# Kernel optimization log

Measured on AMD Instinct MI355X. Metric: run time of the kernel, lower is better.

Reference implementation:

```python
import jax, jax.numpy as jnp
import numpy as np

D_MODEL = 1024
N_HEADS = 16
D_K = D_MODEL // N_HEADS
MAX_POS = 512          # max_position_embeddings; att_span = pos_ebd_size
ATT_SPAN = MAX_POS
B, T = 4, 1024
SCALE_FACTOR = 3       # 1 + c2p + p2c


def setup_inputs() -> dict:
    key = jax.random.key(0)
    ks = jax.random.split(key, 16)
    init = lambda k, shape: (jax.random.normal(k, shape, dtype=jnp.float32) * 0.02)
    inp = {
        "x": jax.random.normal(ks[0], (B, T, D_MODEL), dtype=jnp.float32),
        "Wq": init(ks[1], (D_MODEL, D_MODEL)), "bq": jnp.zeros((D_MODEL,), jnp.float32),
        "Wk": init(ks[2], (D_MODEL, D_MODEL)), "bk": jnp.zeros((D_MODEL,), jnp.float32),
        "Wv": init(ks[3], (D_MODEL, D_MODEL)), "bv": jnp.zeros((D_MODEL,), jnp.float32),
        "Wo": init(ks[4], (D_MODEL, D_MODEL)), "bo": jnp.zeros((D_MODEL,), jnp.float32),
        "Wpk": init(ks[5], (D_MODEL, D_MODEL)), "bpk": jnp.zeros((D_MODEL,), jnp.float32),
        "Wpq": init(ks[6], (D_MODEL, D_MODEL)), "bpq": jnp.zeros((D_MODEL,), jnp.float32),
        "rel_emb": init(ks[7], (2 * ATT_SPAN, D_MODEL)),
    }
    return inp


def _heads(y):
    # (B,T,D) -> (B,H,T,d_k)
    b, t, _ = y.shape
    return y.reshape(b, t, N_HEADS, D_K).transpose(0, 2, 1, 3)


def reference(x, Wq, bq, Wk, bk, Wv, bv, Wo, bo, Wpk, bpk, Wpq, bpq, rel_emb):
    b, t, c = x.shape
    scale = 1.0 / jnp.sqrt(jnp.asarray(D_K * SCALE_FACTOR, x.dtype))

    Q = _heads(x @ Wq.T + bq)  # (B,H,T,d)
    K = _heads(x @ Wk.T + bk)
    V = _heads(x @ Wv.T + bv)

    # relative_position[q,k] = k - q ; rel_pos = clamp(rel + span, 0, 2*span-1)
    rel = jnp.arange(t)[None, :] - jnp.arange(t)[:, None]          # (T,T)
    rel_pos = jnp.clip(rel + ATT_SPAN, 0, 2 * ATT_SPAN - 1)        # c2p index
    p2c_pos = jnp.clip(-rel + ATT_SPAN, 0, 2 * ATT_SPAN - 1)       # p2c index

    # content-to-content
    scores = jnp.einsum('bhqd,bhkd->bhqk', Q, K) * scale

    # c2p: pos_key (2S,H,d) -> per-head scores against Q, then gather over rel_pos
    pos_key = (rel_emb @ Wpk.T + bpk).reshape(2 * ATT_SPAN, N_HEADS, D_K)
    c2p = jnp.einsum('bhqd,shd->bhqs', Q, pos_key) * scale          # (B,H,T,2S)
    c2p = jnp.take_along_axis(c2p, rel_pos[None, None, :, :], axis=-1)  # (B,H,T,T)

    # p2c: pos_query scores against K, gather with p2c_pos, transpose q<->k
    pos_query = (rel_emb @ Wpq.T + bpq).reshape(2 * ATT_SPAN, N_HEADS, D_K)
    p2c = jnp.einsum('bhkd,shd->bhks', K, pos_query) * scale        # (B,H,T,2S)
    p2c = jnp.take_along_axis(p2c, p2c_pos[None, None, :, :], axis=-1)  # (B,H,k,q)
    p2c = jnp.swapaxes(p2c, -1, -2)                                 # (B,H,q,k)

    scores = scores + c2p + p2c
    probs = jax.nn.softmax(scores, axis=-1)
    ctx = jnp.einsum('bhqk,bhkd->bhqd', probs, V)
    ctx = ctx.transpose(0, 2, 1, 3).reshape(b, t, c)
    return ctx @ Wo.T + bo
```

## Files before the change

kernel.cpp:

```cpp
#include <hip/hip_runtime.h>
#include <stdint.h>

typedef __attribute__((ext_vector_type(8))) short bf16x8;
typedef __attribute__((ext_vector_type(4))) float f32x4;

#define DM   1024
#define TT   1024
#define NH   16
#define DKH  64
#define SPAN 512
#define S2   1024
#define MT   4096

__device__ __forceinline__ unsigned short f2b(float f) {
  unsigned int u = __builtin_bit_cast(unsigned int, f);
  u = (u + 0x7FFFu + ((u >> 16) & 1u)) >> 16;
  return (unsigned short)u;
}
__device__ __forceinline__ float b2f(unsigned short h) {
  unsigned int u = ((unsigned int)h) << 16;
  return __builtin_bit_cast(float, u);
}

__device__ __forceinline__ int swz(int row, int col) {
  return (row << 6) + ((((col >> 3) ^ (row & 7)) << 3) | (col & 7));
}

struct CvtArgs {
  const float* src[8];
  unsigned short* dst[8];
  int n[8];
};
__global__ void cvt_multi(CvtArgs a) {
  const int ti = blockIdx.y;
  const float* __restrict__ in = a.src[ti];
  unsigned short* __restrict__ out = a.dst[ti];
  const int n = a.n[ti];
  int i = (blockIdx.x * blockDim.x + threadIdx.x) * 4;
  int stride = gridDim.x * blockDim.x * 4;
  for (; i < n; i += stride) {
    float4 v = *(const float4*)(in + i);
    ushort4 o;
    o.x = f2b(v.x); o.y = f2b(v.y); o.z = f2b(v.z); o.w = f2b(v.w);
    *(ushort4*)(out + i) = o;
  }
}

__global__ __launch_bounds__(256) void gemm_bt(
    const unsigned short* __restrict__ A, const unsigned short* __restrict__ B,
    const float* __restrict__ bias0, const float* __restrict__ bias1, const float* __restrict__ bias2,
    void* __restrict__ C,
    int M, int N, int K, int lda, int ldb, int ldc,
    long long sA, long long sB, long long sC,
    float a0, float a1, float a2, int modes)
{
  __shared__ unsigned short Al[128 * 72];
  __shared__ unsigned short Bl[128 * 72];
  const int t = threadIdx.x;
  const int w = t >> 6, l = t & 63;
  const int g = l >> 4, li = l & 15;
  const int wr = w >> 1, wc = w & 1;
  const int row0 = blockIdx.x * 128, col0 = blockIdx.y * 128;
  const int z = blockIdx.z;
  const unsigned short* Ab = A + (long long)z * sA;
  const unsigned short* Bb = B + (long long)z * sB;

  f32x4 acc[4][4];
#pragma unroll
  for (int m = 0; m < 4; m++)
#pragma unroll
    for (int n = 0; n < 4; n++) acc[m][n] = (f32x4){0.f, 0.f, 0.f, 0.f};

  for (int k0 = 0; k0 < K; k0 += 64) {
    __syncthreads();
#pragma unroll
    for (int i = 0; i < 4; i++) {
      int c = t + 256 * i;
      int r = c >> 3, c8 = (c & 7) * 8;
      *(bf16x8*)&Al[r * 72 + c8] = *(const bf16x8*)&Ab[(long long)(row0 + r) * lda + k0 + c8];
      *(bf16x8*)&Bl[r * 72 + c8] = *(const bf16x8*)&Bb[(long long)(col0 + r) * ldb + k0 + c8];
    }
    __syncthreads();
#pragma unroll
    for (int kk = 0; kk < 2; kk++) {
      bf16x8 af[4], bfr[4];
#pragma unroll
      for (int m = 0; m < 4; m++) af[m]  = *(bf16x8*)&Al[(wr * 64 + m * 16 + li) * 72 + kk * 32 + g * 8];
#pragma unroll
      for (int n = 0; n < 4; n++) bfr[n] = *(bf16x8*)&Bl[(wc * 64 + n * 16 + li) * 72 + kk * 32 + g * 8];
#pragma unroll
      for (int m = 0; m < 4; m++)
#pragma unroll
        for (int n = 0; n < 4; n++)
          acc[m][n] = __builtin_amdgcn_mfma_f32_16x16x32_bf16(af[m], bfr[n], acc[m][n], 0, 0, 0);
    }
  }

  const float alpha = z == 0 ? a0 : (z == 1 ? a1 : a2);
  const float* bias = z == 0 ? bias0 : (z == 1 ? bias1 : bias2);
  const int mode = (modes >> (4 * z)) & 15;
  const long long zoff = (long long)z * sC;

#pragma unroll
  for (int m = 0; m < 4; m++) {
    int row = row0 + wr * 64 + m * 16 + g * 4;
#pragma unroll
    for (int n = 0; n < 4; n++) {
      int col = col0 + wc * 64 + n * 16 + li;
      float bv = bias ? bias[col] : 0.0f;
      if (mode == 2) {
        ushort4 st;
        st.x = f2b((acc[m][n][0] + bv) * alpha);
        st.y = f2b((acc[m][n][1] + bv) * alpha);
        st.z = f2b((acc[m][n][2] + bv) * alpha);
        st.w = f2b((acc[m][n][3] + bv) * alpha);
        *(ushort4*)&((unsigned short*)C)[zoff + (long long)col * M + row] = st;
      } else {
#pragma unroll
        for (int r = 0; r < 4; r++) {
          float v = (acc[m][n][r] + bv) * alpha;
          long long idx = zoff + (long long)(row + r) * ldc + col;
          if (mode == 1) ((unsigned short*)C)[idx] = f2b(v);
          else           ((float*)C)[idx] = v;
        }
      }
    }
  }
}

__global__ __launch_bounds__(256, 3) void attn_fused(
    const unsigned short* __restrict__ Qb, const unsigned short* __restrict__ Kb,
    const unsigned short* __restrict__ VT,
    const unsigned short* __restrict__ PKb, const unsigned short* __restrict__ PQb,
    unsigned short* __restrict__ ctxb)
{
  __shared__ unsigned short Kl[64 * 64];
  __shared__ unsigned short Vtl[64 * 64];
  __shared__ unsigned short Ct[128 * 64];
  __shared__ unsigned short Pq[128 * 64];

  const int t = threadIdx.x, w = t >> 6, l = t & 63, g = l >> 4, li = l & 15;
  const int bid = blockIdx.x;
  const int role = (bid & 7) * 128 + (bid >> 3);
  const int q0 = (role & 15) * 64;
  const int h = (role >> 4) & 15;
  const int b = role >> 8;
  const long long qkbase = ((long long)b * TT) * DM + h * DKH;
  const long long vtb = (long long)(h * DKH) * MT + (long long)b * TT;
  const int hbase = h * DKH;

  bf16x8 aq[2];
#pragma unroll
  for (int kk = 0; kk < 2; kk++)
    aq[kk] = *(const bf16x8*)&Qb[qkbase + (long long)(q0 + w * 16 + li) * DM + kk * 32 + g * 8];

  int w0 = SPAN - q0 - 64;
  w0 = w0 < 0 ? 0 : (w0 > S2 - 128 ? S2 - 128 : w0);
#pragma unroll
  for (int i = 0; i < 4; i++) {
    int c = t + 256 * i;
    int jr = c >> 3, c8 = (c & 7) * 8;
    *(bf16x8*)&Ct[swz((w0 + jr) & 127, c8)] =
        *(const bf16x8*)&PKb[(long long)(w0 + jr) * DM + hbase + c8];
  }
  __syncthreads();
  {
    f32x4 cp[8];
#pragma unroll
    for (int jb = 0; jb < 8; jb++) cp[jb] = (f32x4){0.f, 0.f, 0.f, 0.f};
    __builtin_amdgcn_s_setprio(1);
#pragma unroll
    for (int kk = 0; kk < 2; kk++)
#pragma unroll
      for (int jb = 0; jb < 8; jb++) {
        bf16x8 pkf = *(bf16x8*)&Ct[swz(jb * 16 + li, kk * 32 + g * 8)];
        cp[jb] = __builtin_amdgcn_mfma_f32_16x16x32_bf16(aq[kk], pkf, cp[jb], 0, 0, 0);
      }
    __builtin_amdgcn_s_setprio(0);
    __syncthreads();
#pragma unroll
    for (int jb = 0; jb < 8; jb++) {
      ushort4 a;
      a.x = f2b(cp[jb][0]); a.y = f2b(cp[jb][1]);
      a.z = f2b(cp[jb][2]); a.w = f2b(cp[jb][3]);
      *(ushort4*)&Ct[swz(jb * 16 + li, w * 16 + g * 4)] = a;
    }
  }

  f32x4 o[4];
#pragma unroll
  for (int n = 0; n < 4; n++) o[n] = (f32x4){0.f, 0.f, 0.f, 0.f};
  float mrow[4], lrow[4];
#pragma unroll
  for (int r = 0; r < 4; r++) { mrow[r] = -1e30f; lrow[r] = 0.f; }

  for (int kt = 0; kt < TT / 64; kt++) {
    const int k0 = kt * 64;
    const int d0 = k0 - q0 + SPAN;
    int w0n = d0 - 64;
    w0n = w0n < 0 ? 0 : (w0n > S2 - 128 ? S2 - 128 : w0n);
    const bool slide = (w0n != w0);
    const int sb = w0 & 127;
    const int newrow0 = w0 + 128;
    w0 = w0n;

    __syncthreads();
#pragma unroll
    for (int i = 0; i < 2; i++) {
      int c = t + 256 * i;
      int r = c >> 3, c8 = (c & 7) * 8;
      *(bf16x8*)&Kl[swz(r, c8)]  = *(const bf16x8*)&Kb[qkbase + (long long)(k0 + r) * DM + c8];
      *(bf16x8*)&Vtl[swz(r, c8)] = *(const bf16x8*)&VT[vtb + (long long)r * MT + k0 + c8];
    }
#pragma unroll
    for (int i = 0; i < 4; i++) {
      int c = t + 256 * i;
      int jr = c >> 3, c8 = (c & 7) * 8;
      *(bf16x8*)&Pq[swz(jr, c8)] = *(const bf16x8*)&PQb[(long long)(w0 + jr) * DM + hbase + c8];
    }
    if (slide) {
#pragma unroll
      for (int i = 0; i < 2; i++) {
        int c = t + 256 * i;
        int jr = c >> 3, c8 = (c & 7) * 8;
        *(bf16x8*)&Ct[swz(sb + jr, c8)] =
            *(const bf16x8*)&PKb[(long long)(newrow0 + jr) * DM + hbase + c8];
      }
    }
    __syncthreads();

    bf16x8 ak[2];
#pragma unroll
    for (int kk = 0; kk < 2; kk++) ak[kk] = *(bf16x8*)&Kl[swz(w * 16 + li, kk * 32 + g * 8)];

    __builtin_amdgcn_s_setprio(1);
    f32x4 sc[4];
#pragma unroll
    for (int f = 0; f < 4; f++) sc[f] = (f32x4){0.f, 0.f, 0.f, 0.f};
#pragma unroll
    for (int kk = 0; kk < 2; kk++)
#pragma unroll
      for (int f = 0; f < 4; f++) {
        bf16x8 bk = *(bf16x8*)&Kl[swz(f * 16 + li, kk * 32 + g * 8)];
        sc[f] = __builtin_amdgcn_mfma_f32_16x16x32_bf16(aq[kk], bk, sc[f], 0, 0, 0);
      }
    f32x4 cp2[4];
#pragma unroll
    for (int jb = 0; jb < 4; jb++) cp2[jb] = (f32x4){0.f, 0.f, 0.f, 0.f};
    if (slide) {
#pragma unroll
      for (int kk = 0; kk < 2; kk++)
#pragma unroll
        for (int jb = 0; jb < 4; jb++) {
          bf16x8 pkf = *(bf16x8*)&Ct[swz(sb + jb * 16 + li, kk * 32 + g * 8)];
          cp2[jb] = __builtin_amdgcn_mfma_f32_16x16x32_bf16(aq[kk], pkf, cp2[jb], 0, 0, 0);
        }
    }
    int loA = d0 + w * 16 - 63; loA = loA < w0 ? w0 : loA;
    int hiA = d0 + w * 16 + 15; hiA = hiA > w0 + 127 ? w0 + 127 : hiA;
    const int jb_lo = (loA - w0) >> 4;
    const int jb_n  = ((hiA - w0) >> 4) - jb_lo;
    f32x4 pp[6];
#pragma unroll
    for (int u = 0; u < 6; u++) pp[u] = (f32x4){0.f, 0.f, 0.f, 0.f};
#pragma unroll
    for (int kk = 0; kk < 2; kk++)
#pragma unroll
      for (int u = 0; u < 6; u++)
        if (u <= jb_n) {
          bf16x8 pqf = *(bf16x8*)&Pq[swz((jb_lo + u) * 16 + li, kk * 32 + g * 8)];
          pp[u] = __builtin_amdgcn_mfma_f32_16x16x32_bf16(ak[kk], pqf, pp[u], 0, 0, 0);
        }
    __builtin_amdgcn_s_setprio(0);
    __syncthreads();

    if (slide) {
#pragma unroll
      for (int jb = 0; jb < 4; jb++) {
        ushort4 a;
        a.x = f2b(cp2[jb][0]); a.y = f2b(cp2[jb][1]);
        a.z = f2b(cp2[jb][2]); a.w = f2b(cp2[jb][3]);
        *(ushort4*)&Ct[swz(sb + jb * 16 + li, w * 16 + g * 4)] = a;
      }
    }
#pragma unroll
    for (int u = 0; u < 6; u++)
      if (u <= jb_n) {
        ushort4 a;
        a.x = f2b(pp[u][0]); a.y = f2b(pp[u][1]);
        a.z = f2b(pp[u][2]); a.w = f2b(pp[u][3]);
        *(ushort4*)&Pq[swz((jb_lo + u) * 16 + li, w * 16 + g * 4)] = a;
      }
    __syncthreads();

    float p[4][4];
    float tmax[4] = {-1e30f, -1e30f, -1e30f, -1e30f};
#pragma unroll
    for (int f = 0; f < 4; f++)
#pragma unroll
      for (int r = 0; r < 4; r++) {
        int qi = w * 16 + g * 4 + r;
        int ki = f * 16 + li;
        int sraw = d0 + ki - qi;
        int scl = sraw < 0 ? 0 : (sraw > S2 - 1 ? S2 - 1 : sraw);
        int slot = scl & 127;
        int j = scl - w0;
        float v = sc[f][r] + b2f(Ct[swz(slot, qi)]) + b2f(Pq[swz(j, ki)]);
        p[f][r] = v;
        tmax[r] = fmaxf(tmax[r], v);
      }
#pragma unroll
    for (int msk = 1; msk <= 8; msk <<= 1)
#pragma unroll
      for (int r = 0; r < 4; r++) tmax[r] = fmaxf(tmax[r], __shfl_xor(tmax[r], msk));
    float corr[4];
#pragma unroll
    for (int r = 0; r < 4; r++) {
      float mn = fmaxf(mrow[r], tmax[r]);
      corr[r] = __expf(mrow[r] - mn);
      mrow[r] = mn;
      lrow[r] *= corr[r];
    }
#pragma unroll
    for (int n = 0; n < 4; n++)
#pragma unroll
      for (int r = 0; r < 4; r++) o[n][r] *= corr[r];

    float ps[4] = {0.f, 0.f, 0.f, 0.f};
#pragma unroll
    for (int f = 0; f < 4; f++)
#pragma unroll
      for (int r = 0; r < 4; r++) {
        float e = __expf(p[f][r] - mrow[r]);
        ps[r] += e;
        Kl[swz(w * 16 + g * 4 + r, f * 16 + li)] = f2b(e);
      }
#pragma unroll
    for (int msk = 1; msk <= 8; msk <<= 1)
#pragma unroll
      for (int r = 0; r < 4; r++) ps[r] += __shfl_xor(ps[r], msk);
#pragma unroll
    for (int r = 0; r < 4; r++) lrow[r] += ps[r];

    __builtin_amdgcn_s_setprio(1);
#pragma unroll
    for (int kk = 0; kk < 2; kk++) {
      bf16x8 ap = *(bf16x8*)&Kl[swz(w * 16 + li, kk * 32 + g * 8)];
#pragma unroll
      for (int n = 0; n < 4; n++) {
        bf16x8 bvf = *(bf16x8*)&Vtl[swz(n * 16 + li, kk * 32 + g * 8)];
        o[n] = __builtin_amdgcn_mfma_f32_16x16x32_bf16(ap, bvf, o[n], 0, 0, 0);
      }
    }
    __builtin_amdgcn_s_setprio(0);
  }

#pragma unroll
  for (int n = 0; n < 4; n++)
#pragma unroll
    for (int r = 0; r < 4; r++) {
      int q = q0 + w * 16 + g * 4 + r;
      float val = o[n][r] / lrow[r];
      ctxb[((long long)b * TT + q) * DM + h * DKH + n * 16 + li] = f2b(val);
    }
}

extern "C" void kernel_launch(void* const* d_in, const int* in_sizes, int n_in,
                              void* d_out, int out_size, void* d_ws, size_t ws_size,
                              hipStream_t stream) {
  const float* x   = (const float*)d_in[0];
  const float* Wq  = (const float*)d_in[1];
  const float* bq  = (const float*)d_in[2];
  const float* Wk  = (const float*)d_in[3];
  const float* bk  = (const float*)d_in[4];
  const float* Wv  = (const float*)d_in[5];
  const float* bv  = (const float*)d_in[6];
  const float* Wo  = (const float*)d_in[7];
  const float* bo  = (const float*)d_in[8];
  const float* Wpk = (const float*)d_in[9];
  const float* bpk = (const float*)d_in[10];
  const float* Wpq = (const float*)d_in[11];
  const float* bpq = (const float*)d_in[12];
  const float* rel = (const float*)d_in[13];

  uint8_t* ws = (uint8_t*)d_ws;
  size_t off = 0;
  auto alloc = [&](size_t bytes) -> void* {
    void* p = ws + off;
    off += (bytes + 255) & ~(size_t)255;
    return p;
  };
  unsigned short* xb   = (unsigned short*)alloc((size_t)MT * DM * 2);
  unsigned short* Wqb  = (unsigned short*)alloc((size_t)DM * DM * 2);
  unsigned short* Wkb  = (unsigned short*)alloc((size_t)DM * DM * 2);
  unsigned short* Wvb  = (unsigned short*)alloc((size_t)DM * DM * 2);
  unsigned short* Wob  = (unsigned short*)alloc((size_t)DM * DM * 2);
  unsigned short* Wpkb = (unsigned short*)alloc((size_t)DM * DM * 2);
  unsigned short* Wpqb = (unsigned short*)alloc((size_t)DM * DM * 2);
  unsigned short* reb  = (unsigned short*)alloc((size_t)S2 * DM * 2);
  unsigned short* Qb   = (unsigned short*)alloc((size_t)MT * DM * 2);
  unsigned short* Kb   = (unsigned short*)alloc((size_t)MT * DM * 2);
  unsigned short* VT   = (unsigned short*)alloc((size_t)MT * DM * 2);
  unsigned short* PKb  = (unsigned short*)alloc((size_t)S2 * DM * 2);
  unsigned short* PQb  = (unsigned short*)alloc((size_t)S2 * DM * 2);
  unsigned short* ctxb = (unsigned short*)alloc((size_t)MT * DM * 2);

  const float scale = 0.07216878364870323f;

  CvtArgs ca;
  ca.src[0] = x;   ca.dst[0] = xb;   ca.n[0] = MT * DM;
  ca.src[1] = Wq;  ca.dst[1] = Wqb;  ca.n[1] = DM * DM;
  ca.src[2] = Wk;  ca.dst[2] = Wkb;  ca.n[2] = DM * DM;
  ca.src[3] = Wv;  ca.dst[3] = Wvb;  ca.n[3] = DM * DM;
  ca.src[4] = Wo;  ca.dst[4] = Wob;  ca.n[4] = DM * DM;
  ca.src[5] = Wpk; ca.dst[5] = Wpkb; ca.n[5] = DM * DM;
  ca.src[6] = Wpq; ca.dst[6] = Wpqb; ca.n[6] = DM * DM;
  ca.src[7] = rel; ca.dst[7] = reb;  ca.n[7] = S2 * DM;
  cvt_multi<<<dim3(1024, 8), dim3(256), 0, stream>>>(ca);

  gemm_bt<<<dim3(MT / 128, DM / 128, 3), dim3(256), 0, stream>>>(
      xb, Wqb, bq, bk, bv, Qb,
      MT, DM, DM, DM, DM, DM,
      0, (long long)DM * DM, (long long)MT * DM,
      scale, 1.0f, 1.0f, 0x211);

  gemm_bt<<<dim3(S2 / 128, DM / 128, 2), dim3(256), 0, stream>>>(
      reb, Wpkb, bpk, bpq, nullptr, PKb,
      S2, DM, DM, DM, DM, DM,
      0, (long long)DM * DM, (long long)S2 * DM,
      1.0f, scale, 1.0f, 0x11);

  attn_fused<<<dim3(1024), dim3(256), 0, stream>>>(
      Qb, Kb, VT, PKb, PQb, ctxb);

  gemm_bt<<<dim3(MT / 128, DM / 128, 1), dim3(256), 0, stream>>>(
      ctxb, Wob, bo, nullptr, nullptr, d_out,
      MT, DM, DM, DM, DM, DM,
      0, 0, 0,
      1.0f, 1.0f, 1.0f, 0x0);
}
```

Before: 262.0 us.

## Make attention kernel persistent with atomic work queue and fold log2e into scale

The attention kernel now launches 768 persistent blocks that take their first tile from blockIdx and later tiles from a global atomic counter, which the conversion kernel resets before use. The intent is to smooth out the tail imbalance caused by tiles that do different amounts of sliding-window work. Separately, log2(e) is folded into the Q and position-projection scales so softmax can use exp2f instead of __expf. The queue adds an atomic and an extra barrier per tile, and it depends on the counter being reset by an earlier launch on the same stream.

```diff
diff --git a/kernel.cpp b/kernel.cpp
--- a/kernel.cpp
+++ b/kernel.cpp
@@ -31,7 +31,8 @@
   unsigned short* dst[8];
   int n[8];
 };
-__global__ void cvt_multi(CvtArgs a) {
+__global__ void cvt_multi(CvtArgs a, unsigned int* counter) {
+  if (blockIdx.x == 0 && blockIdx.y == 0 && threadIdx.x == 0) *counter = 768u;
   const int ti = blockIdx.y;
   const float* __restrict__ in = a.src[ti];
   unsigned short* __restrict__ out = a.dst[ti];
@@ -132,237 +133,249 @@
     const unsigned short* __restrict__ Qb, const unsigned short* __restrict__ Kb,
     const unsigned short* __restrict__ VT,
     const unsigned short* __restrict__ PKb, const unsigned short* __restrict__ PQb,
-    unsigned short* __restrict__ ctxb)
+    unsigned short* __restrict__ ctxb, unsigned int* __restrict__ counter)
 {
   __shared__ unsigned short Kl[64 * 64];
   __shared__ unsigned short Vtl[64 * 64];
   __shared__ unsigned short Ct[128 * 64];
   __shared__ unsigned short Pq[128 * 64];
+  __shared__ unsigned int role_sh;
 
   const int t = threadIdx.x, w = t >> 6, l = t & 63, g = l >> 4, li = l & 15;
-  const int bid = blockIdx.x;
-  const int role = (bid & 7) * 128 + (bid >> 3);
-  const int q0 = (role & 15) * 64;
-  const int h = (role >> 4) & 15;
-  const int b = role >> 8;
-  const long long qkbase = ((long long)b * TT) * DM + h * DKH;
-  const long long vtb = (long long)(h * DKH) * MT + (long long)b * TT;
-  const int hbase = h * DKH;
-
-  bf16x8 aq[2];
-#pragma unroll
-  for (int kk = 0; kk < 2; kk++)
-    aq[kk] = *(const bf16x8*)&Qb[qkbase + (long long)(q0 + w * 16 + li) * DM + kk * 32 + g * 8];
-
-  int w0 = SPAN - q0 - 64;
-  w0 = w0 < 0 ? 0 : (w0 > S2 - 128 ? S2 - 128 : w0);
-#pragma unroll
-  for (int i = 0; i < 4; i++) {
-    int c = t + 256 * i;
-    int jr = c >> 3, c8 = (c & 7) * 8;
-    *(bf16x8*)&Ct[swz((w0 + jr) & 127, c8)] =
-        *(const bf16x8*)&PKb[(long long)(w0 + jr) * DM + hbase + c8];
-  }
-  __syncthreads();
-  {
-    f32x4 cp[8];
-#pragma unroll
-    for (int jb = 0; jb < 8; jb++) cp[jb] = (f32x4){0.f, 0.f, 0.f, 0.f};
-    __builtin_amdgcn_s_setprio(1);
+
+  unsigned int idx = blockIdx.x;
+  bool first = true;
+
+  for (;;) {
+    if (!first && t == 0) role_sh = atomicAdd(counter, 1u);
+    __syncthreads();
+    if (!first) idx = role_sh;
+    if (idx >= 1024u) break;
+    first = false;
+
+    const int role = (idx & 7) * 128 + (int)(idx >> 3);
+    const int q0 = (role & 15) * 64;
+    const int h = (role >> 4) & 15;
+    const int b = role >> 8;
+    const long long qkbase = ((long long)b * TT) * DM + h * DKH;
+    const long long vtb = (long long)(h * DKH) * MT + (long long)b * TT;
+    const int hbase = h * DKH;
+
+    bf16x8 aq[2];
 #pragma unroll
     for (int kk = 0; kk < 2; kk++)
-#pragma unroll
-      for (int jb = 0; jb < 8; jb++) {
-        bf16x8 pkf = *(bf16x8*)&Ct[swz(jb * 16 + li, kk * 32 + g * 8)];
-        cp[jb] = __builtin_amdgcn_mfma_f32_16x16x32_bf16(aq[kk], pkf, cp[jb], 0, 0, 0);
-      }
-    __builtin_amdgcn_s_setprio(0);
-    __syncthreads();
-#pragma unroll
-    for (int jb = 0; jb < 8; jb++) {
-      ushort4 a;
-      a.x = f2b(cp[jb][0]); a.y = f2b(cp[jb][1]);
-      a.z = f2b(cp[jb][2]); a.w = f2b(cp[jb][3]);
-      *(ushort4*)&Ct[swz(jb * 16 + li, w * 16 + g * 4)] = a;
-    }
-  }
-
-  f32x4 o[4];
-#pragma unroll
-  for (int n = 0; n < 4; n++) o[n] = (f32x4){0.f, 0.f, 0.f, 0.f};
-  float mrow[4], lrow[4];
-#pragma unroll
-  for (int r = 0; r < 4; r++) { mrow[r] = -1e30f; lrow[r] = 0.f; }
-
-  for (int kt = 0; kt < TT / 64; kt++) {
-    const int k0 = kt * 64;
-    const int d0 = k0 - q0 + SPAN;
-    int w0n = d0 - 64;
-    w0n = w0n < 0 ? 0 : (w0n > S2 - 128 ? S2 - 128 : w0n);
-    const bool slide = (w0n != w0);
-    const int sb = w0 & 127;
-    const int newrow0 = w0 + 128;
-    w0 = w0n;
-
-    __syncthreads();
-#pragma unroll
-    for (int i = 0; i < 2; i++) {
-      int c = t + 256 * i;
-      int r = c >> 3, c8 = (c & 7) * 8;
-      *(bf16x8*)&Kl[swz(r, c8)]  = *(const bf16x8*)&Kb[qkbase + (long long)(k0 + r) * DM + c8];
-      *(bf16x8*)&Vtl[swz(r, c8)] = *(const bf16x8*)&VT[vtb + (long long)r * MT + k0 + c8];
-    }
+      aq[kk] = *(const bf16x8*)&Qb[qkbase + (long long)(q0 + w * 16 + li) * DM + kk * 32 + g * 8];
+
+    int w0 = SPAN - q0 - 64;
+    w0 = w0 < 0 ? 0 : (w0 > S2 - 128 ? S2 - 128 : w0);
 #pragma unroll
     for (int i = 0; i < 4; i++) {
       int c = t + 256 * i;
       int jr = c >> 3, c8 = (c & 7) * 8;
-      *(bf16x8*)&Pq[swz(jr, c8)] = *(const bf16x8*)&PQb[(long long)(w0 + jr) * DM + hbase + c8];
-    }
-    if (slide) {
+      *(bf16x8*)&Ct[swz((w0 + jr) & 127, c8)] =
+          *(const bf16x8*)&PKb[(long long)(w0 + jr) * DM + hbase + c8];
+    }
+    __syncthreads();
+    {
+      f32x4 cp[8];
+#pragma unroll
+      for (int jb = 0; jb < 8; jb++) cp[jb] = (f32x4){0.f, 0.f, 0.f, 0.f};
+      __builtin_amdgcn_s_setprio(1);
+#pragma unroll
+      for (int kk = 0; kk < 2; kk++)
+#pragma unroll
+        for (int jb = 0; jb < 8; jb++) {
+          bf16x8 pkf = *(bf16x8*)&Ct[swz(jb * 16 + li, kk * 32 + g * 8)];
+          cp[jb] = __builtin_amdgcn_mfma_f32_16x16x32_bf16(aq[kk], pkf, cp[jb], 0, 0, 0);
+        }
+      __builtin_amdgcn_s_setprio(0);
+      __syncthreads();
+#pragma unroll
+      for (int jb = 0; jb < 8; jb++) {
+        ushort4 a;
+        a.x = f2b(cp[jb][0]); a.y = f2b(cp[jb][1]);
+        a.z = f2b(cp[jb][2]); a.w = f2b(cp[jb][3]);
+        *(ushort4*)&Ct[swz(jb * 16 + li, w * 16 + g * 4)] = a;
+      }
+    }
+
+    f32x4 o[4];
+#pragma unroll
+    for (int n = 0; n < 4; n++) o[n] = (f32x4){0.f, 0.f, 0.f, 0.f};
+    float mrow[4], lrow[4];
+#pragma unroll
+    for (int r = 0; r < 4; r++) { mrow[r] = -1e30f; lrow[r] = 0.f; }
+
+    for (int kt = 0; kt < TT / 64; kt++) {
+      const int k0 = kt * 64;
+      const int d0 = k0 - q0 + SPAN;
+      int w0n = d0 - 64;
+      w0n = w0n < 0 ? 0 : (w0n > S2 - 128 ? S2 - 128 : w0n);
+      const bool slide = (w0n != w0);
+      const int sb = w0 & 127;
+      const int newrow0 = w0 + 128;
+      w0 = w0n;
+
+      __syncthreads();
 #pragma unroll
       for (int i = 0; i < 2; i++) {
         int c = t + 256 * i;
+        int r = c >> 3, c8 = (c & 7) * 8;
+        *(bf16x8*)&Kl[swz(r, c8)]  = *(const bf16x8*)&Kb[qkbase + (long long)(k0 + r) * DM + c8];
+        *(bf16x8*)&Vtl[swz(r, c8)] = *(const bf16x8*)&VT[vtb + (long long)r * MT + k0 + c8];
+      }
+#pragma unroll
+      for (int i = 0; i < 4; i++) {
+        int c = t + 256 * i;
         int jr = c >> 3, c8 = (c & 7) * 8;
-        *(bf16x8*)&Ct[swz(sb + jr, c8)] =
-            *(const bf16x8*)&PKb[(long long)(newrow0 + jr) * DM + hbase + c8];
-      }
-    }
-    __syncthreads();
-
-    bf16x8 ak[2];
-#pragma unroll
-    for (int kk = 0; kk < 2; kk++) ak[kk] = *(bf16x8*)&Kl[swz(w * 16 + li, kk * 32 + g * 8)];
-
-    __builtin_amdgcn_s_setprio(1);
-    f32x4 sc[4];
-#pragma unroll
-    for (int f = 0; f < 4; f++) sc[f] = (f32x4){0.f, 0.f, 0.f, 0.f};
-#pragma unroll
-    for (int kk = 0; kk < 2; kk++)
-#pragma unroll
-      for (int f = 0; f < 4; f++) {
-        bf16x8 bk = *(bf16x8*)&Kl[swz(f * 16 + li, kk * 32 + g * 8)];
-        sc[f] = __builtin_amdgcn_mfma_f32_16x16x32_bf16(aq[kk], bk, sc[f], 0, 0, 0);
-      }
-    f32x4 cp2[4];
-#pragma unroll
-    for (int jb = 0; jb < 4; jb++) cp2[jb] = (f32x4){0.f, 0.f, 0.f, 0.f};
-    if (slide) {
+        *(bf16x8*)&Pq[swz(jr, c8)] = *(const bf16x8*)&PQb[(long long)(w0 + jr) * DM + hbase + c8];
+      }
+      if (slide) {
+#pragma unroll
+        for (int i = 0; i < 2; i++) {
+          int c = t + 256 * i;
+          int jr = c >> 3, c8 = (c & 7) * 8;
+          *(bf16x8*)&Ct[swz(sb + jr, c8)] =
+              *(const bf16x8*)&PKb[(long long)(newrow0 + jr) * DM + hbase + c8];
+        }
+      }
+      __syncthreads();
+
+      bf16x8 ak[2];
+#pragma unroll
+      for (int kk = 0; kk < 2; kk++) ak[kk] = *(bf16x8*)&Kl[swz(w * 16 + li, kk * 32 + g * 8)];
+
+      __builtin_amdgcn_s_setprio(1);
+      f32x4 sc[4];
+#pragma unroll
+      for (int f = 0; f < 4; f++) sc[f] = (f32x4){0.f, 0.f, 0.f, 0.f};
 #pragma unroll
       for (int kk = 0; kk < 2; kk++)
 #pragma unroll
+        for (int f = 0; f < 4; f++) {
+          bf16x8 bk = *(bf16x8*)&Kl[swz(f * 16 + li, kk * 32 + g * 8)];
+          sc[f] = __builtin_amdgcn_mfma_f32_16x16x32_bf16(aq[kk], bk, sc[f], 0, 0, 0);
+        }
+      f32x4 cp2[4];
+#pragma unroll
+      for (int jb = 0; jb < 4; jb++) cp2[jb] = (f32x4){0.f, 0.f, 0.f, 0.f};
+      if (slide) {
+#pragma unroll
+        for (int kk = 0; kk < 2; kk++)
+#pragma unroll
+          for (int jb = 0; jb < 4; jb++) {
+            bf16x8 pkf = *(bf16x8*)&Ct[swz(sb + jb * 16 + li, kk * 32 + g * 8)];
+            cp2[jb] = __builtin_amdgcn_mfma_f32_16x16x32_bf16(aq[kk], pkf, cp2[jb], 0, 0, 0);
+          }
+      }
+      int loA = d0 + w * 16 - 63; loA = loA < w0 ? w0 : loA;
+      int hiA = d0 + w * 16 + 15; hiA = hiA > w0 + 127 ? w0 + 127 : hiA;
+      const int jb_lo = (loA - w0) >> 4;
+      const int jb_n  = ((hiA - w0) >> 4) - jb_lo;
+      f32x4 pp[6];
+#pragma unroll
+      for (int u = 0; u < 6; u++) pp[u] = (f32x4){0.f, 0.f, 0.f, 0.f};
+#pragma unroll
+      for (int kk = 0; kk < 2; kk++)
+#pragma unroll
+        for (int u = 0; u < 6; u++)
+          if (u <= jb_n) {
+            bf16x8 pqf = *(bf16x8*)&Pq[swz((jb_lo + u) * 16 + li, kk * 32 + g * 8)];
+            pp[u] = __builtin_amdgcn_mfma_f32_16x16x32_bf16(ak[kk], pqf, pp[u], 0, 0, 0);
+          }
+      __builtin_amdgcn_s_setprio(0);
+      __syncthreads();
+
+      if (slide) {
+#pragma unroll
         for (int jb = 0; jb < 4; jb++) {
-          bf16x8 pkf = *(bf16x8*)&Ct[swz(sb + jb * 16 + li, kk * 32 + g * 8)];
-          cp2[jb] = __builtin_amdgcn_mfma_f32_16x16x32_bf16(aq[kk], pkf, cp2[jb], 0, 0, 0);
-        }
-    }
-    int loA = d0 + w * 16 - 63; loA = loA < w0 ? w0 : loA;
-    int hiA = d0 + w * 16 + 15; hiA = hiA > w0 + 127 ? w0 + 127 : hiA;
-    const int jb_lo = (loA - w0) >> 4;
-    const int jb_n  = ((hiA - w0) >> 4) - jb_lo;
-    f32x4 pp[6];
-#pragma unroll
-    for (int u = 0; u < 6; u++) pp[u] = (f32x4){0.f, 0.f, 0.f, 0.f};
-#pragma unroll
-    for (int kk = 0; kk < 2; kk++)
+          ushort4 a;
+          a.x = f2b(cp2[jb][0]); a.y = f2b(cp2[jb][1]);
+          a.z = f2b(cp2[jb][2]); a.w = f2b(cp2[jb][3]);
+          *(ushort4*)&Ct[swz(sb + jb * 16 + li, w * 16 + g * 4)] = a;
+        }
+      }
 #pragma unroll
       for (int u = 0; u < 6; u++)
         if (u <= jb_n) {
-          bf16x8 pqf = *(bf16x8*)&Pq[swz((jb_lo + u) * 16 + li, kk * 32 + g * 8)];
-          pp[u] = __builtin_amdgcn_mfma_f32_16x16x32_bf16(ak[kk], pqf, pp[u], 0, 0, 0);
-        }
-    __builtin_amdgcn_s_setprio(0);
-    __syncthreads();
-
-    if (slide) {
-#pragma unroll
-      for (int jb = 0; jb < 4; jb++) {
-        ushort4 a;
-        a.x = f2b(cp2[jb][0]); a.y = f2b(cp2[jb][1]);
-        a.z = f2b(cp2[jb][2]); a.w = f2b(cp2[jb][3]);
-        *(ushort4*)&Ct[swz(sb + jb * 16 + li, w * 16 + g * 4)] = a;
-      }
-    }
-#pragma unroll
-    for (int u = 0; u < 6; u++)
-      if (u <= jb_n) {
-        ushort4 a;
-        a.x = f2b(pp[u][0]); a.y = f2b(pp[u][1]);
-        a.z = f2b(pp[u][2]); a.w = f2b(pp[u][3]);
-        *(ushort4*)&Pq[swz((jb_lo + u) * 16 + li, w * 16 + g * 4)] = a;
-      }
-    __syncthreads();
-
-    float p[4][4];
-    float tmax[4] = {-1e30f, -1e30f, -1e30f, -1e30f};
-#pragma unroll
-    for (int f = 0; f < 4; f++)
+          ushort4 a;
+          a.x = f2b(pp[u][0]); a.y = f2b(pp[u][1]);
+          a.z = f2b(pp[u][2]); a.w = f2b(pp[u][3]);
+          *(ushort4*)&Pq[swz((jb_lo + u) * 16 + li, w * 16 + g * 4)] = a;
+        }
+      __syncthreads();
+
+      float p[4][4];
+      float tmax[4] = {-1e30f, -1e30f, -1e30f, -1e30f};
+#pragma unroll
+      for (int f = 0; f < 4; f++)
+#pragma unroll
+        for (int r = 0; r < 4; r++) {
+          int qi = w * 16 + g * 4 + r;
+          int ki = f * 16 + li;
+          int sraw = d0 + ki - qi;
+          int scl = sraw < 0 ? 0 : (sraw > S2 - 1 ? S2 - 1 : sraw);
+          int slot = scl & 127;
+          int j = scl - w0;
+          float v = sc[f][r] + b2f(Ct[swz(slot, qi)]) + b2f(Pq[swz(j, ki)]);
+          p[f][r] = v;
+          tmax[r] = fmaxf(tmax[r], v);
+        }
+#pragma unroll
+      for (int msk = 1; msk <= 8; msk <<= 1)
+#pragma unroll
+        for (int r = 0; r < 4; r++) tmax[r] = fmaxf(tmax[r], __shfl_xor(tmax[r], msk));
+      float corr[4];
 #pragma unroll
       for (int r = 0; r < 4; r++) {
-        int qi = w * 16 + g * 4 + r;
-        int ki = f * 16 + li;
-        int sraw = d0 + ki - qi;
-        int scl = sraw < 0 ? 0 : (sraw > S2 - 1 ? S2 - 1 : sraw);
-        int slot = scl & 127;
-        int j = scl - w0;
-        float v = sc[f][r] + b2f(Ct[swz(slot, qi)]) + b2f(Pq[swz(j, ki)]);
-        p[f][r] = v;
-        tmax[r] = fmaxf(tmax[r], v);
-      }
-#pragma unroll
-    for (int msk = 1; msk <= 8; msk <<= 1)
-#pragma unroll
-      for (int r = 0; r < 4; r++) tmax[r] = fmaxf(tmax[r], __shfl_xor(tmax[r], msk));
-    float corr[4];
-#pragma unroll
-    for (int r = 0; r < 4; r++) {
-      float mn = fmaxf(mrow[r], tmax[r]);
-      corr[r] = __expf(mrow[r] - mn);
-      mrow[r] = mn;
-      lrow[r] *= corr[r];
-    }
+        float mn = fmaxf(mrow[r], tmax[r]);
+        corr[r] = exp2f(mrow[r] - mn);
+        mrow[r] = mn;
+        lrow[r] *= corr[r];
+      }
+#pragma unroll
+      for (int n = 0; n < 4; n++)
+#pragma unroll
+        for (int r = 0; r < 4; r++) o[n][r] *= corr[r];
+
+      float ps[4] = {0.f, 0.f, 0.f, 0.f};
+#pragma unroll
+      for (int f = 0; f < 4; f++)
+#pragma unroll
+        for (int r = 0; r < 4; r++) {
+          float e = exp2f(p[f][r] - mrow[r]);
+          ps[r] += e;
+          Kl[swz(w * 16 + g * 4 + r, f * 16 + li)] = f2b(e);
+        }
+#pragma unroll
+      for (int msk = 1; msk <= 8; msk <<= 1)
+#pragma unroll
+        for (int r = 0; r < 4; r++) ps[r] += __shfl_xor(ps[r], msk);
+#pragma unroll
+      for (int r = 0; r < 4; r++) lrow[r] += ps[r];
+
+      __builtin_amdgcn_s_setprio(1);
+#pragma unroll
+      for (int kk = 0; kk < 2; kk++) {
+        bf16x8 ap = *(bf16x8*)&Kl[swz(w * 16 + li, kk * 32 + g * 8)];
+#pragma unroll
+        for (int n = 0; n < 4; n++) {
+          bf16x8 bvf = *(bf16x8*)&Vtl[swz(n * 16 + li, kk * 32 + g * 8)];
+          o[n] = __builtin_amdgcn_mfma_f32_16x16x32_bf16(ap, bvf, o[n], 0, 0, 0);
+        }
+      }
+      __builtin_amdgcn_s_setprio(0);
+    }
+
 #pragma unroll
     for (int n = 0; n < 4; n++)
 #pragma unroll
-      for (int r = 0; r < 4; r++) o[n][r] *= corr[r];
-
-    float ps[4] = {0.f, 0.f, 0.f, 0.f};
-#pragma unroll
-    for (int f = 0; f < 4; f++)
-#pragma unroll
       for (int r = 0; r < 4; r++) {
-        float e = __expf(p[f][r] - mrow[r]);
-        ps[r] += e;
-        Kl[swz(w * 16 + g * 4 + r, f * 16 + li)] = f2b(e);
-      }
-#pragma unroll
-    for (int msk = 1; msk <= 8; msk <<= 1)
-#pragma unroll
-      for (int r = 0; r < 4; r++) ps[r] += __shfl_xor(ps[r], msk);
-#pragma unroll
-    for (int r = 0; r < 4; r++) lrow[r] += ps[r];
-
-    __builtin_amdgcn_s_setprio(1);
-#pragma unroll
-    for (int kk = 0; kk < 2; kk++) {
-      bf16x8 ap = *(bf16x8*)&Kl[swz(w * 16 + li, kk * 32 + g * 8)];
-#pragma unroll
-      for (int n = 0; n < 4; n++) {
-        bf16x8 bvf = *(bf16x8*)&Vtl[swz(n * 16 + li, kk * 32 + g * 8)];
-        o[n] = __builtin_amdgcn_mfma_f32_16x16x32_bf16(ap, bvf, o[n], 0, 0, 0);
-      }
-    }
-    __builtin_amdgcn_s_setprio(0);
+        int q = q0 + w * 16 + g * 4 + r;
+        float val = o[n][r] / lrow[r];
+        ctxb[((long long)b * TT + q) * DM + h * DKH + n * 16 + li] = f2b(val);
+      }
   }
-
-#pragma unroll
-  for (int n = 0; n < 4; n++)
-#pragma unroll
-    for (int r = 0; r < 4; r++) {
-      int q = q0 + w * 16 + g * 4 + r;
-      float val = o[n][r] / lrow[r];
-      ctxb[((long long)b * TT + q) * DM + h * DKH + n * 16 + li] = f2b(val);
-    }
 }
 
 extern "C" void kernel_launch(void* const* d_in, const int* in_sizes, int n_in,
@@ -404,8 +417,9 @@
   unsigned short* PKb  = (unsigned short*)alloc((size_t)S2 * DM * 2);
   unsigned short* PQb  = (unsigned short*)alloc((size_t)S2 * DM * 2);
   unsigned short* ctxb = (unsigned short*)alloc((size_t)MT * DM * 2);
-
-  const float scale = 0.07216878364870323f;
+  unsigned int*   cnt  = (unsigned int*)alloc(256);
+
+  const float scale2 = 0.07216878364870323f * 1.4426950408889634f;
 
   CvtArgs ca;
   ca.src[0] = x;   ca.dst[0] = xb;   ca.n[0] = MT * DM;
@@ -416,22 +430,22 @@
   ca.src[5] = Wpk; ca.dst[5] = Wpkb; ca.n[5] = DM * DM;
   ca.src[6] = Wpq; ca.dst[6] = Wpqb; ca.n[6] = DM * DM;
   ca.src[7] = rel; ca.dst[7] = reb;  ca.n[7] = S2 * DM;
-  cvt_multi<<<dim3(1024, 8), dim3(256), 0, stream>>>(ca);
+  cvt_multi<<<dim3(1024, 8), dim3(256), 0, stream>>>(ca, cnt);
 
   gemm_bt<<<dim3(MT / 128, DM / 128, 3), dim3(256), 0, stream>>>(
       xb, Wqb, bq, bk, bv, Qb,
       MT, DM, DM, DM, DM, DM,
       0, (long long)DM * DM, (long long)MT * DM,
-      scale, 1.0f, 1.0f, 0x211);
+      scale2, 1.0f, 1.0f, 0x211);
 
   gemm_bt<<<dim3(S2 / 128, DM / 128, 2), dim3(256), 0, stream>>>(
       reb, Wpkb, bpk, bpq, nullptr, PKb,
       S2, DM, DM, DM, DM, DM,
       0, (long long)DM * DM, (long long)S2 * DM,
-      1.0f, scale, 1.0f, 0x11);
-
-  attn_fused<<<dim3(1024), dim3(256), 0, stream>>>(
-      Qb, Kb, VT, PKb, PQb, ctxb);
+      1.0f, scale2, 1.0f, 0x11);
+
+  attn_fused<<<dim3(768), dim3(256), 0, stream>>>(
+      Qb, Kb, VT, PKb, PQb, ctxb, cnt);
 
   gemm_bt<<<dim3(MT / 128, DM / 128, 1), dim3(256), 0, stream>>>(
       ctxb, Wob, bo, nullptr, nullptr, d_out,
```

After: 330.9 us. +26.3%, slower.
